# Kernel tuning notes

Hardware: AMD Instinct MI355X
Metric: run time of the kernel (lower is better)

The kernel has to match this reference:

```python
import jax, jax.numpy as jnp
import numpy as np

NUM_EXPERTS = 8
AUX_LOSS_COEF = 0.01


def setup_inputs() -> dict:
    key = jax.random.key(0)
    ks = jax.random.split(key, 5)
    B, S, D, E, H = 4, 2048, 1024, NUM_EXPERTS, 4096
    scale = 0.02  # typical init scale so gelu/softmax stay in sane ranges
    return {
        "hidden_states": jax.random.normal(ks[0], (B, S, D), dtype=jnp.float32),
        "router_w": jax.random.normal(ks[1], (D, E), dtype=jnp.float32) * scale,
        "router_b": jnp.zeros((E,), dtype=jnp.float32),
        "w1": jax.random.normal(ks[2], (E, D, H), dtype=jnp.float32) * scale,
        "b1": jnp.zeros((E, H), dtype=jnp.float32),
        "w2": jax.random.normal(ks[3], (E, H, D), dtype=jnp.float32) * scale,
        "b2": jnp.zeros((E, D), dtype=jnp.float32),
    }


def reference(hidden_states, router_w, router_b, w1, b1, w2, b2):
    B, S, D = hidden_states.shape
    E = w1.shape[0]
    x = hidden_states.reshape(-1, D)  # [T, D] flattened tokens

    # Switch router: top-1 expert, combine weight = softmax prob of chosen expert
    logits = x @ router_w + router_b                      # [T, E]
    probs = jax.nn.softmax(logits, axis=-1)               # [T, E]
    sel = jnp.argmax(logits, axis=-1)                     # [T] int
    gate = jnp.take_along_axis(probs, sel[:, None], axis=1)[:, 0]  # [T]

    # Expert FFNs: per-expert Linear -> gelu -> Linear, masked top-1 combine.
    # Loop is over the small fixed expert count (structurally distinct weights).
    out = jnp.zeros_like(x)
    for e in range(E):
        h = jax.nn.gelu(x @ w1[e] + b1[e])                # [T, H]
        ye = h @ w2[e] + b2[e]                            # [T, D]
        mask = (sel == e).astype(x.dtype)
        out = out + (mask * gate)[:, None] * ye

    # Switch load-balancing auxiliary loss
    mean_probs = probs.mean(axis=0)                       # [E]
    assignments = jnp.mean(jax.nn.one_hot(sel, E, dtype=x.dtype), axis=0)  # [E]
    aux_loss = jnp.sum(mean_probs * assignments) * E
    total_loss = AUX_LOSS_COEF * aux_loss

    return out.reshape(B, S, D), total_loss
```

## Files before the change

kernel.cpp:

```cpp
#include <hip/hip_runtime.h>
#include <cstdint>

typedef __bf16 bf16_t;
typedef __attribute__((ext_vector_type(8))) __bf16 bf16x8;
typedef __attribute__((ext_vector_type(4))) float f32x4;
typedef unsigned short ushort_t;

#define TOKENS 8192
#define DIM 1024
#define HID 4096
#define NEXP 8


__device__ __forceinline__ void gl_lds16(const void* g, void* l) {
  __builtin_amdgcn_global_load_lds(
      (__attribute__((address_space(1))) void*)(void*)g,
      (__attribute__((address_space(3))) void*)l, 16, 0, 0);
}

__device__ __forceinline__ float gelu_fast(float x) {
  float x2 = x * x;
  float z2 = x * (1.59576912f + 0.07135482f * x2);
  float e = __expf(-z2);
  return x * __builtin_amdgcn_rcpf(1.f + e);
}

template <int N>
__device__ __forceinline__ void pwait() {
  __builtin_amdgcn_sched_barrier(0);
  if constexpr (N == 4) asm volatile("s_waitcnt vmcnt(4)" ::: "memory");
  else if constexpr (N == 3) asm volatile("s_waitcnt vmcnt(3)" ::: "memory");
  else asm volatile("s_waitcnt vmcnt(0)" ::: "memory");
  __builtin_amdgcn_sched_barrier(0);
  __builtin_amdgcn_s_barrier();
  __builtin_amdgcn_sched_barrier(0);
}

__device__ __forceinline__ int xcd_chunk(int f, int nwg) {
  int q = nwg >> 3, r = nwg & 7;
  int xcd = f & 7, pos = f >> 3;
  return (xcd < r) ? (xcd * (q + 1) + pos) : (r * (q + 1) + (xcd - r) * q + pos);
}

__global__ void prep_kernel(const float* __restrict__ w1, bf16_t* __restrict__ w1t,
                            const float* __restrict__ x, const float* __restrict__ rw,
                            const float* __restrict__ rbias, bf16_t* __restrict__ xb,
                            int* __restrict__ sel, float* __restrict__ gate,
                            float* __restrict__ pprob, int* __restrict__ pcnt) {
  int bid = blockIdx.x;
  int t = threadIdx.x;
  if (bid < 8192) {
    __shared__ float tile[64][65];
    int e = bid >> 10, xb_ = bid & 1023;
    const float* src = w1 + (size_t)e * DIM * HID;
    bf16_t* dst = w1t + (size_t)e * DIM * HID;
    int rt = xb_ >> 6, ct = xb_ & 63;
    int rb = rt * 64, cb = ct * 64;
    int r = t >> 2, cq = (t & 3) * 16;
    const float* sp = src + (size_t)(rb + r) * HID + cb + cq;
#pragma unroll
    for (int j = 0; j < 16; j += 4) {
      float4 v = *(const float4*)(sp + j);
      tile[r][cq + j + 0] = v.x; tile[r][cq + j + 1] = v.y;
      tile[r][cq + j + 2] = v.z; tile[r][cq + j + 3] = v.w;
    }
    __syncthreads();
    int oc = t >> 2, orr = (t & 3) * 16;
    ushort_t tmp[16];
#pragma unroll
    for (int j = 0; j < 16; ++j) {
      bf16_t b = (bf16_t)tile[orr + j][oc];
      tmp[j] = __builtin_bit_cast(ushort_t, b);
    }
    uint4* dp = (uint4*)(dst + (size_t)(cb + oc) * DIM + rb + orr);
    dp[0] = ((uint4*)tmp)[0];
    dp[1] = ((uint4*)tmp)[1];
  } else {
    __shared__ float sprob[NEXP];
    __shared__ int scnt[NEXP];
    int rblk = bid - 8192;
    int lane = t & 63, wave = t >> 6;
    if (t < NEXP) { sprob[t] = 0.f; scnt[t] = 0; }
    __syncthreads();
    int tok = rblk * 4 + wave;
    const float* xp = x + (size_t)tok * DIM + lane * 16;
    float acc[NEXP];
#pragma unroll
    for (int e = 0; e < NEXP; ++e) acc[e] = 0.f;
    ushort_t xv[16];
#pragma unroll
    for (int j = 0; j < 16; j += 4) {
      float4 v = *(const float4*)(xp + j);
      const float* wr = rw + (size_t)(lane * 16 + j) * NEXP;
      float c[4] = {v.x, v.y, v.z, v.w};
#pragma unroll
      for (int d = 0; d < 4; ++d) {
        xv[j + d] = __builtin_bit_cast(ushort_t, (bf16_t)c[d]);
#pragma unroll
        for (int e = 0; e < NEXP; ++e) acc[e] += c[d] * wr[d * NEXP + e];
      }
    }
    {
      uint4* xop = (uint4*)(xb + (size_t)tok * DIM + lane * 16);
      xop[0] = ((uint4*)xv)[0];
      xop[1] = ((uint4*)xv)[1];
    }
#pragma unroll
    for (int s = 1; s < 64; s <<= 1)
#pragma unroll
      for (int e = 0; e < NEXP; ++e) acc[e] += __shfl_xor(acc[e], s);
    if (lane == 0) {
      float lg[NEXP];
#pragma unroll
      for (int e = 0; e < NEXP; ++e) lg[e] = acc[e] + rbias[e];
      float mx = lg[0]; int am = 0;
#pragma unroll
      for (int e = 1; e < NEXP; ++e) if (lg[e] > mx) { mx = lg[e]; am = e; }
      float p[NEXP]; float se = 0.f;
#pragma unroll
      for (int e = 0; e < NEXP; ++e) { p[e] = __expf(lg[e] - mx); se += p[e]; }
      float inv = 1.f / se;
#pragma unroll
      for (int e = 0; e < NEXP; ++e) { p[e] *= inv; atomicAdd(&sprob[e], p[e]); }
      sel[tok] = am;
      gate[tok] = p[am];
      atomicAdd(&scnt[am], 1);
    }
    __syncthreads();
    if (t < NEXP) {
      pprob[rblk * NEXP + t] = sprob[t];
      pcnt[rblk * NEXP + t] = scnt[t];
    }
  }
}

__global__ void reduce_kernel(const float* __restrict__ pprob, const int* __restrict__ pcnt,
                              int nb, int* __restrict__ meta, float* __restrict__ loss_out) {
  __shared__ float fred[256];
  __shared__ int ired[256];
  int t = threadIdx.x;
  int e = t & 7, i0 = t >> 3;
  float fs = 0.f; int is = 0;
  for (int i = i0; i < nb; i += 32) { fs += pprob[i * 8 + e]; is += pcnt[i * 8 + e]; }
  fred[t] = fs; ired[t] = is;
  __syncthreads();
  if (t < NEXP) {
    float tp = 0.f; int tc = 0;
    for (int j = 0; j < 32; ++j) { tp += fred[j * 8 + t]; tc += ired[j * 8 + t]; }
    meta[t] = tc;
    fred[t] = tp;
    meta[16 + t] = 0;
  }
  __syncthreads();
  if (t == 0) {
    int off = 0; float loss = 0.f; int s1 = 0, s2 = 0;
    for (int q = 0; q < NEXP; ++q) {
      int c = meta[q];
      meta[8 + q] = off;
      int nt1 = (c + 255) >> 8;
      for (int m = 0; m < nt1; ++m) meta[32 + s1++] = (q << 16) | m;
      int nt2 = (c + 127) >> 7;
      for (int m = 0; m < nt2; ++m) meta[96 + s2++] = (q << 16) | m;
      off += c;
      loss += (fred[q] / (float)TOKENS) * ((float)c / (float)TOKENS);
    }
    meta[24] = s1;
    meta[25] = s2;
    *loss_out = loss * (float)NEXP * 0.01f;
  }
}

__global__ void scatter_kernel(const int* __restrict__ sel, int* __restrict__ meta,
                               int* __restrict__ idxl) {
  int tok = blockIdx.x * 256 + threadIdx.x;
  int lane = threadIdx.x & 63;
  int e = sel[tok];
  const int* offsets = meta + 8;
  int* cursors = meta + 16;
#pragma unroll
  for (int ex = 0; ex < NEXP; ++ex) {
    unsigned long long mask = __ballot(e == ex);
    if (e == ex) {
      int leader = __ffsll(mask) - 1;
      int total = __popcll(mask);
      int rank = __popcll(mask & ((1ull << lane) - 1ull));
      int base = 0;
      if (lane == leader) base = atomicAdd(&cursors[ex], total);
      base = __shfl(base, leader);
      idxl[offsets[ex] + base + rank] = tok;
    }
  }
}

#define G1_NWG 1280
#define G1_S 40
#define W2_NBLK 4096

#define STG1(Q, KT) do {                                                     \
    int _kb = (KT) * 32;                                                     \
    gl_lds16(apA0 + _kb, L + (Q) * 12288 + wave * 512);                      \
    gl_lds16(apA1 + _kb, L + (Q) * 12288 + 4096 + wave * 512);               \
    gl_lds16(bpB0 + _kb, L + (Q) * 12288 + 8192 + wave * 512);               \
  } while (0)

#define CMP1(Q) do {                                                         \
    const bf16_t* Ab = L + (Q) * 12288;                                      \
    const bf16_t* Bb = Ab + 8192;                                            \
    bf16x8 af[4], bv[4];                                                     \
    _Pragma("unroll")                                                        \
    for (int m = 0; m < 4; ++m)                                              \
      af[m] = *(const bf16x8*)&Ab[(wrow * 64 + m * 16 + l15) * 32 + ks];     \
    _Pragma("unroll")                                                        \
    for (int n = 0; n < 4; ++n)                                              \
      bv[n] = *(const bf16x8*)&Bb[(wcol * 64 + n * 16 + l15) * 32 + ks];     \
    __builtin_amdgcn_s_setprio(1);                                           \
    _Pragma("unroll")                                                        \
    for (int m = 0; m < 4; ++m)                                              \
      _Pragma("unroll")                                                      \
      for (int n = 0; n < 4; ++n)                                            \
        acc[m][n] = __builtin_amdgcn_mfma_f32_16x16x32_bf16(af[m], bv[n], acc[m][n], 0, 0, 0); \
    __builtin_amdgcn_s_setprio(0);                                           \
  } while (0)

__global__ __launch_bounds__(512, 4) void gemm1_kernel(
    const bf16_t* __restrict__ xb, const bf16_t* __restrict__ w1t,
    const float* __restrict__ b1, const int* __restrict__ idxl,
    const int* __restrict__ meta, bf16_t* __restrict__ h,
    const float* __restrict__ w2, bf16_t* __restrict__ w2t) {
  __shared__ __align__(16) char smemraw[73728];
  int f = blockIdx.x;
  int t = threadIdx.x;

  if (f >= G1_NWG) {
    float (*tile)[65] = (float(*)[65])smemraw;
    int tb = f - G1_NWG;
    int e = tb >> 9, xb_ = tb & 511;
    const float* src = w2 + (size_t)e * HID * DIM;
    bf16_t* dst = w2t + (size_t)e * HID * DIM;
    int rt = xb_ >> 4, ct = xb_ & 15;
    int rb = rt * 128, cb = ct * 64;
    int r = t >> 2, cq = (t & 3) * 16;
    const float* sp = src + (size_t)(rb + r) * DIM + cb + cq;
#pragma unroll
    for (int j = 0; j < 16; j += 4) {
      float4 v = *(const float4*)(sp + j);
      tile[r][cq + j + 0] = v.x; tile[r][cq + j + 1] = v.y;
      tile[r][cq + j + 2] = v.z; tile[r][cq + j + 3] = v.w;
    }
    __syncthreads();
    int oc = t >> 3, orr = (t & 7) * 16;
    ushort_t tmp[16];
#pragma unroll
    for (int j = 0; j < 16; ++j) {
      bf16_t b = (bf16_t)tile[orr + j][oc];
      tmp[j] = __builtin_bit_cast(ushort_t, b);
    }
    uint4* dp = (uint4*)(dst + (size_t)(cb + oc) * HID + rb + orr);
    dp[0] = ((uint4*)tmp)[0];
    dp[1] = ((uint4*)tmp)[1];
    return;
  }

  bf16_t* L = (bf16_t*)smemraw;
  int lf = xcd_chunk(f, G1_NWG);
  int slot = lf % G1_S, nt = lf / G1_S;
  if (slot >= meta[24]) return;
  int tm = meta[32 + slot];
  int e = tm >> 16, mt = tm & 0xffff;
  int cnt = meta[e];
  int off = meta[8 + e];
  int mBase = mt * 256;
  int nBase = nt * 128;
  int lane = t & 63, wave = t >> 6;
  int l15 = lane & 15, g = lane >> 4;
  int wrow = wave >> 1, wcol = wave & 1;
  int ks = (g ^ (l15 & 3)) * 8;
  f32x4 acc[4][4];
#pragma unroll
  for (int m = 0; m < 4; ++m)
#pragma unroll
    for (int n = 0; n < 4; ++n) acc[m][n] = (f32x4){0.f, 0.f, 0.f, 0.f};

  int srow = t >> 2;
  int koff = ((t & 3) ^ (srow & 3)) * 8;
  int c1 = cnt - 1;
  int sA0 = mBase + srow; sA0 = sA0 < c1 ? sA0 : c1;
  int sA1 = mBase + 128 + srow; sA1 = sA1 < c1 ? sA1 : c1;
  const bf16_t* apA0 = xb + (size_t)idxl[off + sA0] * DIM + koff;
  const bf16_t* apA1 = xb + (size_t)idxl[off + sA1] * DIM + koff;
  const bf16_t* wb = w1t + (size_t)e * HID * DIM;
  const bf16_t* bpB0 = wb + (size_t)(nBase + srow) * DIM + koff;

  STG1(0, 0);
  STG1(1, 1);
  pwait<3>();
#pragma unroll 1
  for (int kt = 0; kt < 30; kt += 3) {
    STG1(2, kt + 2); CMP1(0); pwait<3>();
    STG1(0, kt + 3); CMP1(1); pwait<3>();
    STG1(1, kt + 4); CMP1(2); pwait<3>();
  }
  CMP1(0);
  pwait<0>();
  CMP1(1);

  float bias[4];
#pragma unroll
  for (int n = 0; n < 4; ++n) bias[n] = b1[e * HID + nBase + wcol * 64 + n * 16 + l15];
#pragma unroll
  for (int m = 0; m < 4; ++m) {
    int rb0 = mBase + wrow * 64 + m * 16 + g * 4;
#pragma unroll
    for (int j = 0; j < 4; ++j) {
      int r = rb0 + j;
      if (r < cnt) {
        bf16_t* hp = h + (size_t)(off + r) * HID + nBase + wcol * 64 + l15;
#pragma unroll
        for (int n = 0; n < 4; ++n)
          hp[n * 16] = (bf16_t)gelu_fast(acc[m][n][j] + bias[n]);
      }
    }
  }
}

#define STG2(Q, KT) do {                                                     \
    int _kb = (KT) * 32;                                                     \
    gl_lds16(apA0 + _kb, L + (Q) * 8192 + wave * 512);                       \
    gl_lds16(apA1 + _kb, L + (Q) * 8192 + 2048 + wave * 512);                \
    gl_lds16(bpB0 + _kb, L + (Q) * 8192 + 4096 + wave * 512);                \
    gl_lds16(bpB1 + _kb, L + (Q) * 8192 + 6144 + wave * 512);                \
  } while (0)

#define CMP2(Q) do {                                                         \
    const bf16_t* Ab = L + (Q) * 8192;                                       \
    const bf16_t* Bb = Ab + 4096;                                            \
    bf16x8 af[4], bv[4];                                                     \
    _Pragma("unroll")                                                        \
    for (int m = 0; m < 4; ++m)                                              \
      af[m] = *(const bf16x8*)&Ab[(wrow * 64 + m * 16 + l15) * 32 + ks];     \
    _Pragma("unroll")                                                        \
    for (int n = 0; n < 4; ++n)                                              \
      bv[n] = *(const bf16x8*)&Bb[(wcol * 64 + n * 16 + l15) * 32 + ks];     \
    __builtin_amdgcn_s_setprio(1);                                           \
    _Pragma("unroll")                                                        \
    for (int m = 0; m < 4; ++m)                                              \
      _Pragma("unroll")                                                      \
      for (int n = 0; n < 4; ++n)                                            \
        acc[m][n] = __builtin_amdgcn_mfma_f32_16x16x32_bf16(af[m], bv[n], acc[m][n], 0, 0, 0); \
    __builtin_amdgcn_s_setprio(0);                                           \
  } while (0)

__global__ __launch_bounds__(256, 3) void gemm2_kernel(
    const bf16_t* __restrict__ h, const bf16_t* __restrict__ w2t,
    const float* __restrict__ b2, const int* __restrict__ idxl,
    const float* __restrict__ gate, const int* __restrict__ meta,
    float* __restrict__ out) {
  int S = gridDim.x;
  int f = blockIdx.y * S + blockIdx.x;
  int lf = xcd_chunk(f, S * gridDim.y);
  int slot = lf % S, nt = lf / S;
  if (slot >= meta[25]) return;
  int tm = meta[96 + slot];
  int e = tm >> 16, mt = tm & 0xffff;
  int cnt = meta[e];
  int off = meta[8 + e];
  int mBase = mt * 128;
  int nBase = nt * 128;
  __shared__ bf16_t L[24576];
  int t = threadIdx.x, lane = t & 63, wave = t >> 6;
  int l15 = lane & 15, g = lane >> 4;
  int wrow = wave >> 1, wcol = wave & 1;
  int ks = (g ^ (l15 & 3)) * 8;
  f32x4 acc[4][4];
#pragma unroll
  for (int m = 0; m < 4; ++m)
#pragma unroll
    for (int n = 0; n < 4; ++n) acc[m][n] = (f32x4){0.f, 0.f, 0.f, 0.f};

  int srow = t >> 2;
  int koff = ((t & 3) ^ (srow & 3)) * 8;
  int c1 = cnt - 1;
  int sA0 = mBase + srow; sA0 = sA0 < c1 ? sA0 : c1;
  int sA1 = mBase + 64 + srow; sA1 = sA1 < c1 ? sA1 : c1;
  const bf16_t* apA0 = h + (size_t)(off + sA0) * HID + koff;
  const bf16_t* apA1 = h + (size_t)(off + sA1) * HID + koff;
  const bf16_t* wb = w2t + (size_t)e * DIM * HID;
  const bf16_t* bpB0 = wb + (size_t)(nBase + srow) * HID + koff;
  const bf16_t* bpB1 = wb + (size_t)(nBase + 64 + srow) * HID + koff;

  STG2(0, 0);
  STG2(1, 1);
  pwait<4>();
#pragma unroll 1
  for (int kt = 0; kt < 126; kt += 3) {
    STG2(2, kt + 2); CMP2(0); pwait<4>();
    STG2(0, kt + 3); CMP2(1); pwait<4>();
    STG2(1, kt + 4); CMP2(2); pwait<4>();
  }
  CMP2(0);
  pwait<0>();
  CMP2(1);

  float bias[4];
#pragma unroll
  for (int n = 0; n < 4; ++n) bias[n] = b2[e * DIM + nBase + wcol * 64 + n * 16 + l15];
#pragma unroll
  for (int m = 0; m < 4; ++m) {
    int rb0 = mBase + wrow * 64 + m * 16 + g * 4;
#pragma unroll
    for (int j = 0; j < 4; ++j) {
      int r = rb0 + j;
      if (r < cnt) {
        int tok = idxl[off + r];
        float gg = gate[tok];
        float* op = out + (size_t)tok * DIM + nBase + wcol * 64 + l15;
#pragma unroll
        for (int n = 0; n < 4; ++n)
          op[n * 16] = gg * (acc[m][n][j] + bias[n]);
      }
    }
  }
}

extern "C" void kernel_launch(void* const* d_in, const int* in_sizes, int n_in,
                              void* d_out, int out_size, void* d_ws, size_t ws_size,
                              hipStream_t stream) {
  const float* hs = (const float*)d_in[0];
  const float* rw = (const float*)d_in[1];
  const float* rb = (const float*)d_in[2];
  const float* w1 = (const float*)d_in[3];
  const float* b1 = (const float*)d_in[4];
  const float* w2 = (const float*)d_in[5];
  const float* b2 = (const float*)d_in[6];
  float* out = (float*)d_out;
  char* ws = (char*)d_ws;

  bf16_t* xb   = (bf16_t*)(ws + 0);
  bf16_t* w1t  = (bf16_t*)(ws + 16777216);
  bf16_t* w2t  = (bf16_t*)(ws + 83886080);
  bf16_t* hbuf = (bf16_t*)(ws + 150994944);
  int*   sel   = (int*)  (ws + 220200960);
  float* gate  = (float*)(ws + 220233728);
  int*   idxl  = (int*)  (ws + 220266496);
  float* pprob = (float*)(ws + 220299264);
  int*   pcnt  = (int*)  (ws + 220364800);
  int*   meta  = (int*)  (ws + 220430336);

  prep_kernel<<<10240, 256, 0, stream>>>(w1, w1t, hs, rw, rb, xb,
                                         sel, gate, pprob, pcnt);
  reduce_kernel<<<1, 256, 0, stream>>>(pprob, pcnt, 2048, meta, out + (out_size - 1));
  scatter_kernel<<<32, 256, 0, stream>>>(sel, meta, idxl);
  gemm1_kernel<<<G1_NWG + W2_NBLK, 512, 0, stream>>>(xb, w1t, b1, idxl, meta, hbuf,
                                                     w2, w2t);
  gemm2_kernel<<<dim3(72, 8), 256, 0, stream>>>(hbuf, w2t, b2, idxl, gate, meta, out);
}
```

Baseline: 379.3 us.

## Unify both expert GEMMs on a 128x128 four-stage pipelined tile kernel

gemm1 moves from 512-thread 256x128 tiles with a 3-stage ring to 256-thread 128x128 tiles that share gemm2's staging and compute macros. Both GEMMs now use a 4-stage global-to-LDS ring with deeper vmcnt waits, which keeps more loads in flight to hide memory latency. Gemm2's LDS grows to 64KB and its occupancy hint drops to 2 blocks per CU. The w2 transpose blocks are resized to 256 threads, which doubles their count. Smaller gemm1 tiles give more workgroups and better balance, at the cost of more re-reads of the weight and activation tiles.

```diff
diff --git a/kernel.cpp b/kernel.cpp
--- a/kernel.cpp
+++ b/kernel.cpp
@@ -28,8 +28,8 @@
 template <int N>
 __device__ __forceinline__ void pwait() {
   __builtin_amdgcn_sched_barrier(0);
-  if constexpr (N == 4) asm volatile("s_waitcnt vmcnt(4)" ::: "memory");
-  else if constexpr (N == 3) asm volatile("s_waitcnt vmcnt(3)" ::: "memory");
+  if constexpr (N == 8) asm volatile("s_waitcnt vmcnt(8)" ::: "memory");
+  else if constexpr (N == 4) asm volatile("s_waitcnt vmcnt(4)" ::: "memory");
   else asm volatile("s_waitcnt vmcnt(0)" ::: "memory");
   __builtin_amdgcn_sched_barrier(0);
   __builtin_amdgcn_s_barrier();
@@ -192,138 +192,7 @@
   }
 }
 
-#define G1_NWG 1280
-#define G1_S 40
-#define W2_NBLK 4096
-
-#define STG1(Q, KT) do {                                                     \
-    int _kb = (KT) * 32;                                                     \
-    gl_lds16(apA0 + _kb, L + (Q) * 12288 + wave * 512);                      \
-    gl_lds16(apA1 + _kb, L + (Q) * 12288 + 4096 + wave * 512);               \
-    gl_lds16(bpB0 + _kb, L + (Q) * 12288 + 8192 + wave * 512);               \
-  } while (0)
-
-#define CMP1(Q) do {                                                         \
-    const bf16_t* Ab = L + (Q) * 12288;                                      \
-    const bf16_t* Bb = Ab + 8192;                                            \
-    bf16x8 af[4], bv[4];                                                     \
-    _Pragma("unroll")                                                        \
-    for (int m = 0; m < 4; ++m)                                              \
-      af[m] = *(const bf16x8*)&Ab[(wrow * 64 + m * 16 + l15) * 32 + ks];     \
-    _Pragma("unroll")                                                        \
-    for (int n = 0; n < 4; ++n)                                              \
-      bv[n] = *(const bf16x8*)&Bb[(wcol * 64 + n * 16 + l15) * 32 + ks];     \
-    __builtin_amdgcn_s_setprio(1);                                           \
-    _Pragma("unroll")                                                        \
-    for (int m = 0; m < 4; ++m)                                              \
-      _Pragma("unroll")                                                      \
-      for (int n = 0; n < 4; ++n)                                            \
-        acc[m][n] = __builtin_amdgcn_mfma_f32_16x16x32_bf16(af[m], bv[n], acc[m][n], 0, 0, 0); \
-    __builtin_amdgcn_s_setprio(0);                                           \
-  } while (0)
-
-__global__ __launch_bounds__(512, 4) void gemm1_kernel(
-    const bf16_t* __restrict__ xb, const bf16_t* __restrict__ w1t,
-    const float* __restrict__ b1, const int* __restrict__ idxl,
-    const int* __restrict__ meta, bf16_t* __restrict__ h,
-    const float* __restrict__ w2, bf16_t* __restrict__ w2t) {
-  __shared__ __align__(16) char smemraw[73728];
-  int f = blockIdx.x;
-  int t = threadIdx.x;
-
-  if (f >= G1_NWG) {
-    float (*tile)[65] = (float(*)[65])smemraw;
-    int tb = f - G1_NWG;
-    int e = tb >> 9, xb_ = tb & 511;
-    const float* src = w2 + (size_t)e * HID * DIM;
-    bf16_t* dst = w2t + (size_t)e * HID * DIM;
-    int rt = xb_ >> 4, ct = xb_ & 15;
-    int rb = rt * 128, cb = ct * 64;
-    int r = t >> 2, cq = (t & 3) * 16;
-    const float* sp = src + (size_t)(rb + r) * DIM + cb + cq;
-#pragma unroll
-    for (int j = 0; j < 16; j += 4) {
-      float4 v = *(const float4*)(sp + j);
-      tile[r][cq + j + 0] = v.x; tile[r][cq + j + 1] = v.y;
-      tile[r][cq + j + 2] = v.z; tile[r][cq + j + 3] = v.w;
-    }
-    __syncthreads();
-    int oc = t >> 3, orr = (t & 7) * 16;
-    ushort_t tmp[16];
-#pragma unroll
-    for (int j = 0; j < 16; ++j) {
-      bf16_t b = (bf16_t)tile[orr + j][oc];
-      tmp[j] = __builtin_bit_cast(ushort_t, b);
-    }
-    uint4* dp = (uint4*)(dst + (size_t)(cb + oc) * HID + rb + orr);
-    dp[0] = ((uint4*)tmp)[0];
-    dp[1] = ((uint4*)tmp)[1];
-    return;
-  }
-
-  bf16_t* L = (bf16_t*)smemraw;
-  int lf = xcd_chunk(f, G1_NWG);
-  int slot = lf % G1_S, nt = lf / G1_S;
-  if (slot >= meta[24]) return;
-  int tm = meta[32 + slot];
-  int e = tm >> 16, mt = tm & 0xffff;
-  int cnt = meta[e];
-  int off = meta[8 + e];
-  int mBase = mt * 256;
-  int nBase = nt * 128;
-  int lane = t & 63, wave = t >> 6;
-  int l15 = lane & 15, g = lane >> 4;
-  int wrow = wave >> 1, wcol = wave & 1;
-  int ks = (g ^ (l15 & 3)) * 8;
-  f32x4 acc[4][4];
-#pragma unroll
-  for (int m = 0; m < 4; ++m)
-#pragma unroll
-    for (int n = 0; n < 4; ++n) acc[m][n] = (f32x4){0.f, 0.f, 0.f, 0.f};
-
-  int srow = t >> 2;
-  int koff = ((t & 3) ^ (srow & 3)) * 8;
-  int c1 = cnt - 1;
-  int sA0 = mBase + srow; sA0 = sA0 < c1 ? sA0 : c1;
-  int sA1 = mBase + 128 + srow; sA1 = sA1 < c1 ? sA1 : c1;
-  const bf16_t* apA0 = xb + (size_t)idxl[off + sA0] * DIM + koff;
-  const bf16_t* apA1 = xb + (size_t)idxl[off + sA1] * DIM + koff;
-  const bf16_t* wb = w1t + (size_t)e * HID * DIM;
-  const bf16_t* bpB0 = wb + (size_t)(nBase + srow) * DIM + koff;
-
-  STG1(0, 0);
-  STG1(1, 1);
-  pwait<3>();
-#pragma unroll 1
-  for (int kt = 0; kt < 30; kt += 3) {
-    STG1(2, kt + 2); CMP1(0); pwait<3>();
-    STG1(0, kt + 3); CMP1(1); pwait<3>();
-    STG1(1, kt + 4); CMP1(2); pwait<3>();
-  }
-  CMP1(0);
-  pwait<0>();
-  CMP1(1);
-
-  float bias[4];
-#pragma unroll
-  for (int n = 0; n < 4; ++n) bias[n] = b1[e * HID + nBase + wcol * 64 + n * 16 + l15];
-#pragma unroll
-  for (int m = 0; m < 4; ++m) {
-    int rb0 = mBase + wrow * 64 + m * 16 + g * 4;
-#pragma unroll
-    for (int j = 0; j < 4; ++j) {
-      int r = rb0 + j;
-      if (r < cnt) {
-        bf16_t* hp = h + (size_t)(off + r) * HID + nBase + wcol * 64 + l15;
-#pragma unroll
-        for (int n = 0; n < 4; ++n)
-          hp[n * 16] = (bf16_t)gelu_fast(acc[m][n][j] + bias[n]);
-      }
-    }
-  }
-}
-
-#define STG2(Q, KT) do {                                                     \
+#define STG(Q, KT) do {                                                      \
     int _kb = (KT) * 32;                                                     \
     gl_lds16(apA0 + _kb, L + (Q) * 8192 + wave * 512);                       \
     gl_lds16(apA1 + _kb, L + (Q) * 8192 + 2048 + wave * 512);                \
@@ -331,7 +200,7 @@
     gl_lds16(bpB1 + _kb, L + (Q) * 8192 + 6144 + wave * 512);                \
   } while (0)
 
-#define CMP2(Q) do {                                                         \
+#define CMP(Q) do {                                                          \
     const bf16_t* Ab = L + (Q) * 8192;                                       \
     const bf16_t* Bb = Ab + 4096;                                            \
     bf16x8 af[4], bv[4];                                                     \
@@ -350,7 +219,117 @@
     __builtin_amdgcn_s_setprio(0);                                           \
   } while (0)
 
-__global__ __launch_bounds__(256, 3) void gemm2_kernel(
+#define PIPE(NT) do {                                                        \
+    STG(0, 0); STG(1, 1); STG(2, 2);                                         \
+    pwait<8>();                                                              \
+    _Pragma("unroll 1")                                                      \
+    for (int kt = 0; kt < (NT) - 4; kt += 4) {                               \
+      STG(3, kt + 3); CMP(0); pwait<8>();                                    \
+      STG(0, kt + 4); CMP(1); pwait<8>();                                    \
+      STG(1, kt + 5); CMP(2); pwait<8>();                                    \
+      STG(2, kt + 6); CMP(3); pwait<8>();                                    \
+    }                                                                        \
+    STG(3, (NT) - 1); CMP(0); pwait<8>();                                    \
+    CMP(1); pwait<4>();                                                      \
+    CMP(2); pwait<0>();                                                      \
+    CMP(3);                                                                  \
+  } while (0)
+
+#define G1_NWG 2304
+#define W2_NBLK 8192
+
+__global__ __launch_bounds__(256, 2) void gemm1_kernel(
+    const bf16_t* __restrict__ xb, const bf16_t* __restrict__ w1t,
+    const float* __restrict__ b1, const int* __restrict__ idxl,
+    const int* __restrict__ meta, bf16_t* __restrict__ h,
+    const float* __restrict__ w2, bf16_t* __restrict__ w2t) {
+  __shared__ __align__(16) char smemraw[65536];
+  int f = blockIdx.x;
+  int t = threadIdx.x;
+
+  if (f >= G1_NWG) {
+    float (*tile)[65] = (float(*)[65])smemraw;
+    int tb = f - G1_NWG;
+    int e = tb >> 10, xb_ = tb & 1023;
+    const float* src = w2 + (size_t)e * HID * DIM;
+    bf16_t* dst = w2t + (size_t)e * HID * DIM;
+    int rt = xb_ >> 4, ct = xb_ & 15;
+    int rb = rt * 64, cb = ct * 64;
+    int r = t >> 2, cq = (t & 3) * 16;
+    const float* sp = src + (size_t)(rb + r) * DIM + cb + cq;
+#pragma unroll
+    for (int j = 0; j < 16; j += 4) {
+      float4 v = *(const float4*)(sp + j);
+      tile[r][cq + j + 0] = v.x; tile[r][cq + j + 1] = v.y;
+      tile[r][cq + j + 2] = v.z; tile[r][cq + j + 3] = v.w;
+    }
+    __syncthreads();
+    int oc = t >> 2, orr = (t & 3) * 16;
+    ushort_t tmp[16];
+#pragma unroll
+    for (int j = 0; j < 16; ++j) {
+      bf16_t b = (bf16_t)tile[orr + j][oc];
+      tmp[j] = __builtin_bit_cast(ushort_t, b);
+    }
+    uint4* dp = (uint4*)(dst + (size_t)(cb + oc) * HID + rb + orr);
+    dp[0] = ((uint4*)tmp)[0];
+    dp[1] = ((uint4*)tmp)[1];
+    return;
+  }
+
+  bf16_t* L = (bf16_t*)smemraw;
+  int lf = xcd_chunk(f, G1_NWG);
+  int slot = lf % 72, nt = lf / 72;
+  if (slot >= meta[25]) return;
+  int tm = meta[96 + slot];
+  int e = tm >> 16, mt = tm & 0xffff;
+  int cnt = meta[e];
+  int off = meta[8 + e];
+  int mBase = mt * 128;
+  int nBase = nt * 128;
+  int lane = t & 63, wave = t >> 6;
+  int l15 = lane & 15, g = lane >> 4;
+  int wrow = wave >> 1, wcol = wave & 1;
+  int ks = (g ^ (l15 & 3)) * 8;
+  f32x4 acc[4][4];
+#pragma unroll
+  for (int m = 0; m < 4; ++m)
+#pragma unroll
+    for (int n = 0; n < 4; ++n) acc[m][n] = (f32x4){0.f, 0.f, 0.f, 0.f};
+
+  int srow = t >> 2;
+  int koff = ((t & 3) ^ (srow & 3)) * 8;
+  int c1 = cnt - 1;
+  int sA0 = mBase + srow; sA0 = sA0 < c1 ? sA0 : c1;
+  int sA1 = mBase + 64 + srow; sA1 = sA1 < c1 ? sA1 : c1;
+  const bf16_t* apA0 = xb + (size_t)idxl[off + sA0] * DIM + koff;
+  const bf16_t* apA1 = xb + (size_t)idxl[off + sA1] * DIM + koff;
+  const bf16_t* wb = w1t + (size_t)e * HID * DIM;
+  const bf16_t* bpB0 = wb + (size_t)(nBase + srow) * DIM + koff;
+  const bf16_t* bpB1 = wb + (size_t)(nBase + 64 + srow) * DIM + koff;
+
+  PIPE(32);
+
+  float bias[4];
+#pragma unroll
+  for (int n = 0; n < 4; ++n) bias[n] = b1[e * HID + nBase + wcol * 64 + n * 16 + l15];
+#pragma unroll
+  for (int m = 0; m < 4; ++m) {
+    int rb0 = mBase + wrow * 64 + m * 16 + g * 4;
+#pragma unroll
+    for (int j = 0; j < 4; ++j) {
+      int r = rb0 + j;
+      if (r < cnt) {
+        bf16_t* hp = h + (size_t)(off + r) * HID + nBase + wcol * 64 + l15;
+#pragma unroll
+        for (int n = 0; n < 4; ++n)
+          hp[n * 16] = (bf16_t)gelu_fast(acc[m][n][j] + bias[n]);
+      }
+    }
+  }
+}
+
+__global__ __launch_bounds__(256, 2) void gemm2_kernel(
     const bf16_t* __restrict__ h, const bf16_t* __restrict__ w2t,
     const float* __restrict__ b2, const int* __restrict__ idxl,
     const float* __restrict__ gate, const int* __restrict__ meta,
@@ -366,7 +345,7 @@
   int off = meta[8 + e];
   int mBase = mt * 128;
   int nBase = nt * 128;
-  __shared__ bf16_t L[24576];
+  __shared__ bf16_t L[32768];
   int t = threadIdx.x, lane = t & 63, wave = t >> 6;
   int l15 = lane & 15, g = lane >> 4;
   int wrow = wave >> 1, wcol = wave & 1;
@@ -388,18 +367,7 @@
   const bf16_t* bpB0 = wb + (size_t)(nBase + srow) * HID + koff;
   const bf16_t* bpB1 = wb + (size_t)(nBase + 64 + srow) * HID + koff;
 
-  STG2(0, 0);
-  STG2(1, 1);
-  pwait<4>();
-#pragma unroll 1
-  for (int kt = 0; kt < 126; kt += 3) {
-    STG2(2, kt + 2); CMP2(0); pwait<4>();
-    STG2(0, kt + 3); CMP2(1); pwait<4>();
-    STG2(1, kt + 4); CMP2(2); pwait<4>();
-  }
-  CMP2(0);
-  pwait<0>();
-  CMP2(1);
+  PIPE(128);
 
   float bias[4];
 #pragma unroll
@@ -450,7 +418,7 @@
                                          sel, gate, pprob, pcnt);
   reduce_kernel<<<1, 256, 0, stream>>>(pprob, pcnt, 2048, meta, out + (out_size - 1));
   scatter_kernel<<<32, 256, 0, stream>>>(sel, meta, idxl);
-  gemm1_kernel<<<G1_NWG + W2_NBLK, 512, 0, stream>>>(xb, w1t, b1, idxl, meta, hbuf,
+  gemm1_kernel<<<G1_NWG + W2_NBLK, 256, 0, stream>>>(xb, w1t, b1, idxl, meta, hbuf,
                                                      w2, w2t);
   gemm2_kernel<<<dim3(72, 8), 256, 0, stream>>>(hbuf, w2t, b2, idxl, gate, meta, out);
 }
```

Measured after the change: 385.6 us. No clear change (+1.7%).
